# Performance work log

Measured on AMD Instinct MI355X. Metric: run time of the kernel, lower is better.

The kernel has to match this reference:

```python
import jax, jax.numpy as jnp
import numpy as np

EPS = 1e-5
K_NBR = 21   # num_neighbors + 1 (self)
PSI = 4


def _bn(x, g, b):
    # BatchNorm (training-mode forward): channel-last, normalize over all other axes
    axes = tuple(range(x.ndim - 1))
    m = jnp.mean(x, axis=axes, keepdims=True)
    v = jnp.var(x, axis=axes, keepdims=True)
    return (x - m) * jax.lax.rsqrt(v + EPS) * g + b


def setup_inputs() -> dict:
    key = jax.random.key(0)
    ks = jax.random.split(key, 16)
    B, N, Cin, Cout = 4, 2048, 64, 256
    h = Cout // 2
    w_ch = Cout // PSI
    heads = 2 * PSI - 1

    def w(k, o, i):
        return jax.random.normal(k, (o, i), dtype=jnp.float32) * (1.0 / np.sqrt(i))

    p = {}
    p['xyz'] = jax.random.normal(ks[0], (B, N, 3), dtype=jnp.float32)
    p['f'] = jax.random.normal(ks[1], (B, Cin, N), dtype=jnp.float32)
    p['W_geo'] = w(ks[2], h, 6);       p['g_geo'] = jnp.ones(h);   p['b_geo'] = jnp.zeros(h)
    p['W_feat'] = w(ks[3], h, 2 * Cin); p['g_feat'] = jnp.ones(h); p['b_feat'] = jnp.zeros(h)
    p['g_bn'] = jnp.ones(Cout); p['b_bn'] = jnp.zeros(Cout)
    p['W_q'] = w(ks[4], Cout, Cout); p['g_q'] = jnp.ones(Cout); p['b_q'] = jnp.zeros(Cout)
    p['W_k'] = w(ks[5], Cout, Cout); p['g_k'] = jnp.ones(Cout); p['b_k'] = jnp.zeros(Cout)
    p['W_v'] = w(ks[6], Cout, Cout); p['g_v'] = jnp.ones(Cout); p['b_v'] = jnp.zeros(Cout)
    p['W_fus'] = w(ks[7], Cout, heads * w_ch); p['bias_fus'] = jnp.zeros(Cout)
    p['g_fus'] = jnp.ones(Cout); p['b_fus'] = jnp.zeros(Cout)
    p['g_ln'] = jnp.ones(Cout); p['b_ln'] = jnp.zeros(Cout)
    p['W_mlp'] = w(ks[8], Cout, Cout); p['bias_mlp'] = jnp.zeros(Cout)
    return p


def reference(xyz, f, W_geo, g_geo, b_geo, W_feat, g_feat, b_feat, g_bn, b_bn,
              W_q, g_q, b_q, W_k, g_k, b_k, W_v, g_v, b_v,
              W_fus, bias_fus, g_fus, b_fus, g_ln, b_ln, W_mlp, bias_mlp):
    B, N, _ = xyz.shape
    Cout = g_bn.shape[0]
    w_ch = Cout // PSI
    d_sh = w_ch // 2
    heads = 2 * PSI - 1

    # ---- PositionFusion: KNN grouping ----
    sq = jnp.sum(xyz * xyz, axis=-1)                                   # [B,N]
    d2 = sq[:, :, None] + sq[:, None, :] - 2.0 * jnp.einsum('bnd,bmd->bnm', xyz, xyz)
    _, idx = jax.lax.top_k(-d2, K_NBR)                                 # [B,N,K]

    grouped_xyz = jax.vmap(lambda p, i: p[i])(xyz, idx)                # [B,N,K,3]
    xyz_diff = grouped_xyz - xyz[:, :, None, :]
    geo_in = jnp.concatenate(
        [jnp.broadcast_to(xyz[:, :, None, :], grouped_xyz.shape), xyz_diff], axis=-1)  # [B,N,K,6]

    ft = jnp.transpose(f, (0, 2, 1))                                   # [B,N,Cin]
    grouped_f = jax.vmap(lambda p, i: p[i])(ft, idx)                   # [B,N,K,Cin]
    feat_in = jnp.concatenate(
        [grouped_f, jnp.broadcast_to(ft[:, :, None, :], grouped_f.shape)], axis=-1)    # [B,N,K,2Cin]

    geo = jax.nn.relu(_bn(jnp.einsum('bnki,oi->bnko', geo_in, W_geo), g_geo, b_geo))
    fea = jax.nn.relu(_bn(jnp.einsum('bnki,oi->bnko', feat_in, W_feat), g_feat, b_feat))
    feature_ = jnp.max(jnp.concatenate([geo, fea], axis=-1), axis=2)   # [B,N,Cout] (maxpool over K)

    # ---- BatchNorm1d ----
    x = _bn(feature_, g_bn, b_bn)

    # ---- Shifted-channel multi-head attention ----
    q = jax.nn.relu(_bn(jnp.einsum('bnc,oc->bno', x, W_q), g_q, b_q))
    k = jax.nn.relu(_bn(jnp.einsum('bnc,oc->bno', x, W_k), g_k, b_k))
    v = jax.nn.relu(_bn(jnp.einsum('bnc,oc->bno', x, W_v), g_v, b_v))

    qh = jnp.stack([q[..., m * d_sh:m * d_sh + w_ch] for m in range(heads)], axis=1)  # [B,H,N,w]
    kh = jnp.stack([k[..., m * d_sh:m * d_sh + w_ch] for m in range(heads)], axis=1)
    vh = jnp.stack([v[..., m * d_sh:m * d_sh + w_ch] for m in range(heads)], axis=1)

    a = jax.nn.softmax(jnp.einsum('bhnc,bhmc->bhnm', qh, kh), axis=-1)  # [B,H,N,N]
    o = jnp.einsum('bhnm,bhmc->bhnc', a, vh)                            # [B,H,N,w]
    O = jnp.transpose(o, (0, 2, 1, 3)).reshape(B, N, heads * w_ch)      # channel-concat per head

    fus = jax.nn.relu(_bn(jnp.einsum('bnc,oc->bno', O, W_fus) + bias_fus, g_fus, b_fus))

    feature__ = fus + feature_                                          # residual

    # ---- LayerNorm over channels ----
    m = jnp.mean(feature__, axis=-1, keepdims=True)
    var = jnp.var(feature__, axis=-1, keepdims=True)
    y = (feature__ - m) * jax.lax.rsqrt(var + EPS) * g_ln + b_ln

    out = feature__ + (jnp.einsum('bnc,oc->bno', y, W_mlp) + bias_mlp)
    return jnp.transpose(out, (0, 2, 1))                                # [B,Cout,N] like torch
```

## Files before the change

kernel.cpp:

```cpp
#include <hip/hip_runtime.h>
#include <math.h>

#define NB    4
#define NPTS  2048
#define ROWS  (NB*NPTS)
#define CIN   64
#define COUT  256
#define KNBR  21
#define NHEADS 7
#define WCH   64
#define DSH   32
#define LOG2E 1.4426950408889634f
#define KLD   72

typedef __attribute__((ext_vector_type(8))) short short8;
typedef __attribute__((ext_vector_type(4))) float floatx4;

#if __has_builtin(__builtin_amdgcn_exp2f)
#define EXP2(x) __builtin_amdgcn_exp2f(x)
#else
#define EXP2(x) __expf((x)*0.6931471805599453f)
#endif
#if __has_builtin(__builtin_amdgcn_rcpf)
#define RCP(x) __builtin_amdgcn_rcpf(x)
#else
#define RCP(x) (1.0f/(x))
#endif

__device__ __forceinline__ ushort f2bf(float x) {
    unsigned u = __float_as_uint(x);
    u += 0x7fffu + ((u >> 16) & 1u);
    return (ushort)(u >> 16);
}

__device__ __forceinline__ float bf2f(short u) {
    return __uint_as_float(((unsigned)(unsigned short)u) << 16);
}

__device__ __forceinline__ unsigned cvt_pk_bf16(float lo, float hi) {
    unsigned r;
    asm("v_cvt_pk_bf16_f32 %0, %1, %2" : "=v"(r) : "v"(lo), "v"(hi));
    return r;
}

template<int CTRL, int RMASK>
__device__ __forceinline__ unsigned dpp_umin_step(unsigned x) {
    unsigned t = (unsigned)__builtin_amdgcn_update_dpp((int)x, (int)x, CTRL, RMASK, 0xF, false);
    return (t < x) ? t : x;
}
__device__ __forceinline__ unsigned wave_min_u32(unsigned x) {
    x = dpp_umin_step<0x111, 0xF>(x);
    x = dpp_umin_step<0x112, 0xF>(x);
    x = dpp_umin_step<0x114, 0xF>(x);
    x = dpp_umin_step<0x118, 0xF>(x);
    x = dpp_umin_step<0x142, 0xA>(x);
    x = dpp_umin_step<0x143, 0xC>(x);
    return (unsigned)__builtin_amdgcn_readlane((int)x, 63);
}

__device__ __forceinline__ unsigned umin2(unsigned a, unsigned b) { return a < b ? a : b; }
__device__ __forceinline__ unsigned umax2(unsigned a, unsigned b) { return a < b ? b : a; }

__device__ __forceinline__ void ins6(unsigned &m1, unsigned &m2, unsigned &m3,
                                     unsigned &m4, unsigned &m5, unsigned &m6, unsigned k) {
    unsigned c = k, t;
    t = umin2(m1, c); c = umax2(m1, c); m1 = t;
    t = umin2(m2, c); c = umax2(m2, c); m2 = t;
    t = umin2(m3, c); c = umax2(m3, c); m3 = t;
    t = umin2(m4, c); c = umax2(m4, c); m4 = t;
    t = umin2(m5, c); c = umax2(m5, c); m5 = t;
    m6 = umin2(m6, c);
}

__global__ __launch_bounds__(256) void prep_knn(const float* __restrict__ f, const float* __restrict__ Wf,
                                                const float* __restrict__ xyz, const float* __restrict__ Wg,
                                                const float* __restrict__ W_q, const float* __restrict__ W_k,
                                                const float* __restrict__ W_v, const float* __restrict__ W_fus,
                                                float* __restrict__ X, float* __restrict__ A,
                                                ushort* __restrict__ Wb, float* __restrict__ sums,
                                                int* __restrict__ idx) {
    __shared__ float4 SXQ[2048];
    int t = threadIdx.x;
    int blk = blockIdx.x;
    if (blk < 512) {
        float* As = (float*)SXQ;
        float* Ws = As + 16*68;
        int bx = blk & 127, by = blk >> 7;
        if (by == 0 && bx < 12) sums[bx*256 + t] = 0.f;
        int gid = (by*128 + bx)*256 + t;
        for (int i = gid; i < 311296; i += 131072) {
            const float* Wsrc; int off;
            if (i < 65536)       { Wsrc = W_q;   off = i; }
            else if (i < 131072) { Wsrc = W_k;   off = i - 65536; }
            else if (i < 196608) { Wsrc = W_v;   off = i - 131072; }
            else                 { Wsrc = W_fus; off = i - 196608; }
            Wb[i] = f2bf(Wsrc[off]);
        }
        int r0 = bx * 64, n0 = by * 64;
        for (int e = t; e < 4096; e += 256) {
            int row = r0 + (e >> 6), c = n0 + (e & 63), cc = c & 127;
            float x = xyz[row*3], y = xyz[row*3+1], z = xyz[row*3+2];
            const float* w = Wg + cc*6;
            float s = (c < 128) ? ((w[3]*x + w[4]*y) + w[5]*z)
                                : (((w[0]-w[3])*x + (w[1]-w[4])*y) + (w[2]-w[5])*z);
            A[(size_t)row*256 + c] = s;
        }
        int b = r0 >> 11, nbase = r0 & 2047;
        int tx = t & 15, ty = t >> 4;
        float acc[4][4];
#pragma unroll
        for (int i = 0; i < 4; i++)
#pragma unroll
            for (int j = 0; j < 4; j++) acc[i][j] = 0.f;
        int m64 = t & 63, kg = t >> 6;
        int lk = t & 15, lm = t >> 4;
        for (int k0 = 0; k0 < 64; k0 += 16) {
#pragma unroll
            for (int p = 0; p < 4; p++) {
                int k = kg*4 + p;
                As[k*68 + m64] = f[(size_t)b*CIN*NPTS + (size_t)(k0 + k)*NPTS + nbase + m64];
            }
#pragma unroll
            for (int i2 = 0; i2 < 4; i2++) {
                int cg = n0 + lm + 16*i2;
                Ws[lk*68 + lm + 16*i2] = Wf[(size_t)(cg & 127)*128 + (cg >> 7)*64 + k0 + lk];
            }
            __syncthreads();
#pragma unroll
            for (int kq = 0; kq < 16; kq++) {
                float4 a  = *(const float4*)&As[kq*68 + 4*ty];
                float4 b4 = *(const float4*)&Ws[kq*68 + 4*tx];
                float av[4] = {a.x, a.y, a.z, a.w};
                float bv[4] = {b4.x, b4.y, b4.z, b4.w};
#pragma unroll
                for (int i = 0; i < 4; i++)
#pragma unroll
                    for (int j = 0; j < 4; j++) acc[i][j] = fmaf(av[i], bv[j], acc[i][j]);
            }
            __syncthreads();
        }
#pragma unroll
        for (int i = 0; i < 4; i++)
#pragma unroll
            for (int j = 0; j < 4; j++)
                X[(size_t)(r0 + 4*ty + i)*256 + n0 + 4*tx + j] = acc[i][j];
        return;
    }
    int kb = blk - 512;
    int b = kb >> 9;
    int g = kb & 511;
    for (int m = t; m < NPTS; m += 256) {
        float x = xyz[(size_t)b*NPTS*3 + m*3];
        float y = xyz[(size_t)b*NPTS*3 + m*3 + 1];
        float z = xyz[(size_t)b*NPTS*3 + m*3 + 2];
        SXQ[m] = make_float4(x, y, z, (x*x + y*y) + z*z);
    }
    __syncthreads();
    int w = t >> 6, lane = t & 63;
    int n = g*4 + w;
    float4 q4 = SXQ[n];
    float qx = q4.x, qy = q4.y, qz = q4.z, sqn = q4.w;

    unsigned key[32];
    unsigned a1 = 0xFFFFFFFFu, a2 = 0xFFFFFFFFu, a3 = 0xFFFFFFFFu,
             a4 = 0xFFFFFFFFu, a5 = 0xFFFFFFFFu, a6 = 0xFFFFFFFFu;
    unsigned c1 = 0xFFFFFFFFu, c2 = 0xFFFFFFFFu, c3 = 0xFFFFFFFFu,
             c4 = 0xFFFFFFFFu, c5 = 0xFFFFFFFFu, c6 = 0xFFFFFFFFu;
#pragma unroll
    for (int i = 0; i < 16; i++) {
        int m = lane + (i << 6);
        float4 p = SXQ[m];
        float dt = (qx*p.x + qy*p.y) + qz*p.z;
        float d2 = fmaxf((sqn + p.w) - 2.0f*dt, 0.f);
        unsigned kv = (__float_as_uint(d2) & 0xFFFFF800u) | (unsigned)m;
        key[i] = kv;
        ins6(a1, a2, a3, a4, a5, a6, kv);
    }
#pragma unroll
    for (int i = 16; i < 32; i++) {
        int m = lane + (i << 6);
        float4 p = SXQ[m];
        float dt = (qx*p.x + qy*p.y) + qz*p.z;
        float d2 = fmaxf((sqn + p.w) - 2.0f*dt, 0.f);
        unsigned kv = (__float_as_uint(d2) & 0xFFFFF800u) | (unsigned)m;
        key[i] = kv;
        ins6(c1, c2, c3, c4, c5, c6, kv);
    }
    ins6(a1, a2, a3, a4, a5, a6, c1);
    ins6(a1, a2, a3, a4, a5, a6, c2);
    ins6(a1, a2, a3, a4, a5, a6, c3);
    ins6(a1, a2, a3, a4, a5, a6, c4);
    ins6(a1, a2, a3, a4, a5, a6, c5);
    ins6(a1, a2, a3, a4, a5, a6, c6);

    unsigned winkey = 0xFFFFFFFFu;
    {
        unsigned fr = a1, p2 = a2, p3 = a3, p4 = a4, p5 = a5, p6 = a6;
#pragma unroll
        for (int kk = 0; kk < 32; kk++) {
            unsigned win = wave_min_u32(fr);
            if (lane == kk) winkey = win;
            bool own = (fr == win);
            fr = own ? p2 : fr;
            p2 = own ? p3 : p2;
            p3 = own ? p4 : p3;
            p4 = own ? p5 : p4;
            p5 = own ? p6 : p5;
            p6 = own ? 0xFFFFFFFFu : p6;
        }
        if (__ballot(fr == 0xFFFFFFFFu) != 0ULL) {
            winkey = 0xFFFFFFFFu;
            for (int kk = 0; kk < 32; kk++) {
                unsigned lv = key[0];
#pragma unroll
                for (int i = 1; i < 32; i++) lv = (key[i] < lv) ? key[i] : lv;
                unsigned win = wave_min_u32(lv);
                if (lane == kk) winkey = win;
                unsigned widx = win & 2047u;
                int slot = (int)(widx >> 6);
                bool own = (lane == (int)(widx & 63u));
#pragma unroll
                for (int i = 0; i < 32; i++)
                    if (i == slot && own) key[i] = 0xFFFFFFFFu;
            }
        }
    }
    double d2r;
    int mr;
    {
        double qx64 = (double)qx, qy64 = (double)qy, qz64 = (double)qz;
        double sqn64 = qx64*qx64 + qy64*qy64 + qz64*qz64;
        if (lane < 32) {
            mr = (int)(winkey & 2047u);
            float4 p = SXQ[mr];
            double x = (double)p.x, y = (double)p.y, z = (double)p.z;
            double sqm = x*x + y*y + z*z;
            double dt  = qx64*x + qy64*y + qz64*z;
            d2r = (sqn64 + sqm) - 2.0*dt;
        } else {
            d2r = INFINITY; mr = 0x7FFFFFFF;
        }
    }
#pragma unroll
    for (int k = 2; k <= 32; k <<= 1) {
#pragma unroll
        for (int j = k >> 1; j > 0; j >>= 1) {
            double od = __shfl_xor(d2r, j, 64);
            int    om = __shfl_xor(mr, j, 64);
            bool up    = ((lane & k) == 0);
            bool lower = ((lane & j) == 0);
            bool oless = (od < d2r) || (od == d2r && om < mr);
            bool keepOther = up ? (lower ? oless : !oless) : (lower ? !oless : oless);
            if (keepOther) { d2r = od; mr = om; }
        }
    }
    if (lane < KNBR)
        idx[((size_t)b*NPTS + n)*KNBR + lane] = mr;
}

__global__ __launch_bounds__(256) void stats_gf(const float* __restrict__ geoBC, const float* __restrict__ featAC,
                                                const int* __restrict__ idx, const float* __restrict__ g_geo,
                                                const float* __restrict__ g_feat,
                                                float* __restrict__ sums, float* __restrict__ xsel) {
    int c = threadIdx.x;
    int cc = c & 127;
    const float* base = (c < 128) ? geoBC : featAC;
    bool wantmax = ((c < 128) ? g_geo[cc] : g_feat[cc]) >= 0.f;
    float s = 0.f, ss = 0.f;
    int r0 = blockIdx.x * 32;
    for (int r = r0; r < r0 + 32; r++) {
        int b = r >> 11;
        float ctr = base[(size_t)r*256 + 128 + cc];
        float mx = -1e30f, mn = 1e30f;
        const int* ip = idx + (size_t)r*KNBR;
        for (int kk = 0; kk < KNBR; kk++) {
            int j = ip[kk];
            float xv = ctr + base[((size_t)(b*NPTS + j))*256 + cc];
            mx = fmaxf(mx, xv); mn = fminf(mn, xv);
            s += xv; ss += xv*xv;
        }
        xsel[(size_t)r*256 + c] = wantmax ? mx : mn;
    }
    atomicAdd(&sums[c], s);
    atomicAdd(&sums[256 + c], ss);
}

__global__ __launch_bounds__(256) void feature_maxsel(const float* __restrict__ xsel, const float* __restrict__ sums,
                                                      const float* __restrict__ g_geo, const float* __restrict__ b_geo,
                                                      const float* __restrict__ g_feat, const float* __restrict__ b_feat,
                                                      float* __restrict__ feat, float* __restrict__ sums_bn1) {
    int c = threadIdx.x;
    const float inv = 1.0f / (float)(ROWS*KNBR);
    float mean = sums[c]*inv;
    float var  = sums[256+c]*inv - mean*mean;
    float g  = (c < 128) ? g_geo[c] : g_feat[c-128];
    float bb = (c < 128) ? b_geo[c] : b_feat[c-128];
    float sc = g / sqrtf(var + 1e-5f);
    float tt = bb - mean*sc;
    float s = 0.f, ss = 0.f;
    int r0 = blockIdx.x*32;
    for (int r = r0; r < r0+32; r++) {
        size_t i = (size_t)r*256 + c;
        float y = fmaxf(fmaf(sc, xsel[i], tt), 0.f);
        feat[i] = y; s += y; ss += y*y;
    }
    atomicAdd(&sums_bn1[c], s); atomicAdd(&sums_bn1[256+c], ss);
}

__global__ __launch_bounds__(256) void gemm_qkv(const float* __restrict__ Af, const float* __restrict__ sums_in,
                                                const float* __restrict__ g_bn, const float* __restrict__ b_bn,
                                                const ushort* __restrict__ Wb,
                                                float* __restrict__ QKVF, float* __restrict__ sums) {
    __shared__ float bns[2][256];
    __shared__ float red[4][256][2];
    int t = threadIdx.x;
    int r0 = blockIdx.x * 64, g = blockIdx.y;
    int w = t >> 6, lane = t & 63;
    int r15 = lane & 15, quad = lane >> 4;
    {
        float mean = sums_in[512 + t] * (1.0f/(float)ROWS);
        float var  = sums_in[768 + t] * (1.0f/(float)ROWS) - mean*mean;
        float sc = g_bn[t] / sqrtf(var + 1e-5f);
        bns[0][t] = sc;
        bns[1][t] = b_bn[t] - mean*sc;
    }
    __syncthreads();
    short8 aq[8];
    {
        const float* ap = Af + (size_t)(r0 + 16*w + r15)*256;
#pragma unroll
        for (int kc = 0; kc < 8; kc++) {
            int k0 = 32*kc + 8*quad;
            float4 a0 = *(const float4*)&ap[k0];
            float4 a1 = *(const float4*)&ap[k0+4];
            float4 s0 = *(const float4*)&bns[0][k0];
            float4 s1 = *(const float4*)&bns[0][k0+4];
            float4 h0 = *(const float4*)&bns[1][k0];
            float4 h1 = *(const float4*)&bns[1][k0+4];
            ushort u8[8];
            u8[0] = f2bf(fmaf(s0.x, a0.x, h0.x)); u8[1] = f2bf(fmaf(s0.y, a0.y, h0.y));
            u8[2] = f2bf(fmaf(s0.z, a0.z, h0.z)); u8[3] = f2bf(fmaf(s0.w, a0.w, h0.w));
            u8[4] = f2bf(fmaf(s1.x, a1.x, h1.x)); u8[5] = f2bf(fmaf(s1.y, a1.y, h1.y));
            u8[6] = f2bf(fmaf(s1.z, a1.z, h1.z)); u8[7] = f2bf(fmaf(s1.w, a1.w, h1.w));
            aq[kc] = *(short8*)u8;
        }
    }
    floatx4 zero4 = {0.f, 0.f, 0.f, 0.f};
    floatx4 acc[16];
#pragma unroll
    for (int st = 0; st < 16; st++) acc[st] = zero4;
    const ushort* wbase = Wb + (size_t)g*65536 + (size_t)r15*256 + 8*quad;
#pragma unroll
    for (int st = 0; st < 16; st++) {
        const ushort* wp = wbase + (size_t)(16*st)*256;
#pragma unroll
        for (int kc = 0; kc < 8; kc++) {
            short8 bf = *(const short8*)(wp + 32*kc);
            acc[st] = __builtin_amdgcn_mfma_f32_16x16x32_bf16(aq[kc], bf, acc[st], 0, 0, 0);
        }
    }
#pragma unroll
    for (int st = 0; st < 16; st++) {
        float s  = (acc[st][0] + acc[st][1]) + (acc[st][2] + acc[st][3]);
        float q2 = (acc[st][0]*acc[st][0] + acc[st][1]*acc[st][1]) +
                   (acc[st][2]*acc[st][2] + acc[st][3]*acc[st][3]);
        s  += __shfl_xor(s, 16, 64);  s  += __shfl_xor(s, 32, 64);
        q2 += __shfl_xor(q2, 16, 64); q2 += __shfl_xor(q2, 32, 64);
        if (lane < 16) { red[w][16*st + r15][0] = s; red[w][16*st + r15][1] = q2; }
#pragma unroll
        for (int reg = 0; reg < 4; reg++)
            QKVF[(size_t)(r0 + 16*w + 4*quad + reg)*768 + g*256 + 16*st + r15] = acc[st][reg];
    }
    __syncthreads();
    {
        float s = red[0][t][0] + red[1][t][0] + red[2][t][0] + red[3][t][0];
        float q = red[0][t][1] + red[1][t][1] + red[2][t][1] + red[3][t][1];
        atomicAdd(&sums[1024 + g*512 + t], s);
        atomicAdd(&sums[1024 + g*512 + 256 + t], q);
    }
}

__global__ __launch_bounds__(256) void affine_qkv(const float* __restrict__ QKVF, const float* __restrict__ sums,
                                                  const float* __restrict__ g_q, const float* __restrict__ b_q,
                                                  const float* __restrict__ g_k, const float* __restrict__ b_k,
                                                  const float* __restrict__ g_v, const float* __restrict__ b_v,
                                                  ushort* __restrict__ qk, ushort* __restrict__ vt) {
    __shared__ float sts[6][256];
    __shared__ ushort tile[64][72];
    int t = threadIdx.x;
    {
        const float* gs[3] = {g_q, g_k, g_v};
        const float* bs[3] = {b_q, b_k, b_v};
#pragma unroll
        for (int g = 0; g < 3; g++) {
            float mean = sums[1024 + g*512 + t] * (1.0f/(float)ROWS);
            float var  = sums[1024 + g*512 + 256 + t] * (1.0f/(float)ROWS) - mean*mean;
            float sc = gs[g][t] / sqrtf(var + 1e-5f);
            float sh = bs[g][t] - mean*sc;
            if (g == 0) { sc *= LOG2E; sh *= LOG2E; }
            sts[2*g][t] = sc;
            sts[2*g+1][t] = sh;
        }
    }
    __syncthreads();
    int r0 = blockIdx.x * 64, c0 = blockIdx.y * 64;
    int b = r0 >> 11, nbase = r0 & 2047;
    if (c0 < 512) {
#pragma unroll
        for (int rep = 0; rep < 16; rep++) {
            int e = t + 256*rep;
            int row = e >> 6, c = e & 63;
            int col = c0 + c, g = col >> 8, cc = col & 255;
            float v = QKVF[(size_t)(r0 + row)*768 + col];
            v = fmaxf(fmaf(sts[2*g][cc], v, sts[2*g+1][cc]), 0.f);
            qk[(size_t)(r0 + row)*512 + col] = f2bf(v);
        }
    } else {
#pragma unroll
        for (int rep = 0; rep < 16; rep++) {
            int e = t + 256*rep;
            int row = e >> 6, c = e & 63;
            int col = c0 + c, cc = col & 255;
            float v = QKVF[(size_t)(r0 + row)*768 + col];
            v = fmaxf(fmaf(sts[4][cc], v, sts[5][cc]), 0.f);
            tile[c][row] = f2bf(v);
        }
        __syncthreads();
#pragma unroll
        for (int rep = 0; rep < 16; rep++) {
            int e = t + 256*rep;
            int cc = e >> 6, nn = e & 63;
            vt[((size_t)(b*256 + (c0 - 512) + cc))*2048 + nbase + nn] = tile[cc][nn];
        }
    }
}

__global__ __launch_bounds__(512) void attn2(const ushort* __restrict__ qk, const ushort* __restrict__ vt,
                                             ushort* __restrict__ obp, float* __restrict__ ml) {
    __shared__ ushort Ksh[2][64*KLD];
    __shared__ ushort Vts[2][64*KLD];
    int h = blockIdx.y;
    int z = blockIdx.z, b = z >> 1, half = z & 1;
    int r0 = blockIdx.x * 128;
    int t = threadIdx.x;
    int w = t >> 6, lane = t & 63;
    int r15 = lane & 15, quad = lane >> 4;
    size_t rowbase = (size_t)b*NPTS;
    int hoff = h*DSH;
    int rr = t >> 3, c8 = t & 7;
    int mstart = half << 10, mend = mstart + 1024;

    const ushort* ksrc = qk + (rowbase + rr)*512 + 256 + hoff + 8*c8;
    const ushort* vsrc = vt + ((size_t)(b*256 + hoff + rr))*2048 + 8*c8;
    int ldstK = rr*KLD + 8*c8;
    int vb = 4*((c8 >> 1) & 1) + 16*(c8 & 1) + 32*(c8 >> 2);
    int ldstV = rr*KLD + vb;

    short8 aq[2];
#pragma unroll
    for (int s = 0; s < 2; s++)
        aq[s] = *(const short8*)(qk + (rowbase + r0 + 16*w + r15)*512 + hoff + 32*s + 8*quad);

    {
        uint4 k0 = *(const uint4*)(ksrc + (size_t)mstart*512);
        uint4 v0 = *(const uint4*)(vsrc + mstart);
        *(uint4*)&Ksh[0][ldstK] = k0;
        *(uint2*)&Vts[0][ldstV]     = make_uint2(v0.x, v0.y);
        *(uint2*)&Vts[0][ldstV + 8] = make_uint2(v0.z, v0.w);
    }

    floatx4 zero4 = {0.f, 0.f, 0.f, 0.f};
    floatx4 oacc[4];
    float mrun = -1e30f, lrun = 0.f;
#pragma unroll
    for (int i = 0; i < 4; i++) oacc[i] = zero4;

    asm volatile("s_waitcnt lgkmcnt(0)" ::: "memory");
    __builtin_amdgcn_s_barrier();
    __builtin_amdgcn_sched_barrier(0);

    int cur = 0;
    for (int m0 = mstart; m0 < mend; m0 += 64) {
        int mnext = (m0 + 64 < mend) ? (m0 + 64) : mstart;
        uint4 kreg = *(const uint4*)(ksrc + (size_t)mnext*512);
        uint4 vreg = *(const uint4*)(vsrc + mnext);

        const ushort* Kc = Ksh[cur];
        const ushort* Vc = Vts[cur];

        floatx4 sacc[4];
#pragma unroll
        for (int tt = 0; tt < 4; tt++) sacc[tt] = zero4;
        __builtin_amdgcn_s_setprio(1);
#pragma unroll
        for (int tt = 0; tt < 4; tt++) {
            int key = 16*tt + r15;
#pragma unroll
            for (int s = 0; s < 2; s++) {
                short8 kf = *(const short8*)&Kc[key*KLD + 32*s + 8*quad];
                sacc[tt] = __builtin_amdgcn_mfma_f32_16x16x32_bf16(kf, aq[s], sacc[tt], 0, 0, 0);
            }
        }
        __builtin_amdgcn_s_setprio(0);

        float mx = sacc[0][0];
#pragma unroll
        for (int tt = 0; tt < 4; tt++)
#pragma unroll
            for (int reg = 0; reg < 4; reg++) mx = fmaxf(mx, sacc[tt][reg]);
        mx = fmaxf(mx, __shfl_xor(mx, 16, 64));
        mx = fmaxf(mx, __shfl_xor(mx, 32, 64));

        if (!__all(mx <= mrun)) {
            float mnew = fmaxf(mrun, mx);
            float alpha = EXP2(mrun - mnew);
            lrun *= alpha;
#pragma unroll
            for (int td = 0; td < 4; td++) oacc[td] *= alpha;
            mrun = mnew;
        }

        float pm[4][4];
        float rs = 0.f;
#pragma unroll
        for (int tt = 0; tt < 4; tt++) {
#pragma unroll
            for (int reg = 0; reg < 4; reg++) {
                float p = EXP2(sacc[tt][reg] - mrun);
                pm[tt][reg] = p; rs += p;
            }
        }
        rs += __shfl_xor(rs, 16, 64);
        rs += __shfl_xor(rs, 32, 64);
        lrun += rs;

        uint4 pk0, pk1;
        pk0.x = cvt_pk_bf16(pm[0][0], pm[0][1]); pk0.y = cvt_pk_bf16(pm[0][2], pm[0][3]);
        pk0.z = cvt_pk_bf16(pm[1][0], pm[1][1]); pk0.w = cvt_pk_bf16(pm[1][2], pm[1][3]);
        pk1.x = cvt_pk_bf16(pm[2][0], pm[2][1]); pk1.y = cvt_pk_bf16(pm[2][2], pm[2][3]);
        pk1.z = cvt_pk_bf16(pm[3][0], pm[3][1]); pk1.w = cvt_pk_bf16(pm[3][2], pm[3][3]);
        short8 pf0 = *(short8*)&pk0;
        short8 pf1 = *(short8*)&pk1;

        __builtin_amdgcn_s_setprio(1);
#pragma unroll
        for (int td = 0; td < 4; td++) {
            short8 vf0 = *(const short8*)&Vc[(16*td + r15)*KLD + 8*quad];
            oacc[td] = __builtin_amdgcn_mfma_f32_16x16x32_bf16(vf0, pf0, oacc[td], 0, 0, 0);
            short8 vf1 = *(const short8*)&Vc[(16*td + r15)*KLD + 32 + 8*quad];
            oacc[td] = __builtin_amdgcn_mfma_f32_16x16x32_bf16(vf1, pf1, oacc[td], 0, 0, 0);
        }
        __builtin_amdgcn_s_setprio(0);

        *(uint4*)&Ksh[cur ^ 1][ldstK] = kreg;
        *(uint2*)&Vts[cur ^ 1][ldstV]     = make_uint2(vreg.x, vreg.y);
        *(uint2*)&Vts[cur ^ 1][ldstV + 8] = make_uint2(vreg.z, vreg.w);
        cur ^= 1;

        asm volatile("s_waitcnt lgkmcnt(0)" ::: "memory");
        __builtin_amdgcn_s_barrier();
        __builtin_amdgcn_sched_barrier(0);
    }

    size_t grow = rowbase + r0 + 16*w + r15;
    ushort* op = obp + (size_t)half*((size_t)ROWS*448) + grow*448 + h*WCH;
#pragma unroll
    for (int td = 0; td < 4; td++) {
        uint2 o2;
        o2.x = cvt_pk_bf16(oacc[td][0], oacc[td][1]);
        o2.y = cvt_pk_bf16(oacc[td][2], oacc[td][3]);
        *(uint2*)&op[16*td + 4*quad] = o2;
    }
    if (quad == 0) {
        *(float2*)&ml[(grow*7 + h)*4 + half*2] = make_float2(mrun, lrun);
    }
}

__global__ __launch_bounds__(256) void gemm_fus(const ushort* __restrict__ OBP, const float* __restrict__ ML,
                                                const ushort* __restrict__ Wb,
                                                const float* __restrict__ bias, float* __restrict__ C,
                                                float* __restrict__ sums) {
    __shared__ float red[4][128][2];
    int t = threadIdx.x;
    int r0 = blockIdx.x * 64, n0 = blockIdx.y * 128;
    int w = t >> 6, lane = t & 63;
    int r15 = lane & 15, quad = lane >> 4;
    int arow = 16*w + r15;
    short8 aq[14];
    {
        const ushort* p1 = OBP + (size_t)(r0 + arow)*448;
        const ushort* p2 = p1 + (size_t)ROWS*448;
        const float* mlr = ML + (size_t)(r0 + arow)*28;
        float w1[7], w2[7];
#pragma unroll
        for (int hh = 0; hh < 7; hh++) {
            float m1 = mlr[hh*4+0], l1 = mlr[hh*4+1];
            float m2 = mlr[hh*4+2], l2 = mlr[hh*4+3];
            float M  = fmaxf(m1, m2);
            float e1 = EXP2(m1 - M), e2 = EXP2(m2 - M);
            float inv = RCP(fmaf(e1, l1, e2*l2));
            w1[hh] = e1*inv; w2[hh] = e2*inv;
        }
#pragma unroll
        for (int kc = 0; kc < 14; kc++) {
            int k0 = 32*kc + 8*quad;
            short8 a1 = *(const short8*)(p1 + k0);
            short8 a2 = *(const short8*)(p2 + k0);
            const int hh = kc >> 1;
            float c0 = fmaf(w1[hh], bf2f(a1[0]), w2[hh]*bf2f(a2[0]));
            float c1 = fmaf(w1[hh], bf2f(a1[1]), w2[hh]*bf2f(a2[1]));
            float c2 = fmaf(w1[hh], bf2f(a1[2]), w2[hh]*bf2f(a2[2]));
            float c3 = fmaf(w1[hh], bf2f(a1[3]), w2[hh]*bf2f(a2[3]));
            float c4 = fmaf(w1[hh], bf2f(a1[4]), w2[hh]*bf2f(a2[4]));
            float c5 = fmaf(w1[hh], bf2f(a1[5]), w2[hh]*bf2f(a2[5]));
            float c6 = fmaf(w1[hh], bf2f(a1[6]), w2[hh]*bf2f(a2[6]));
            float c7 = fmaf(w1[hh], bf2f(a1[7]), w2[hh]*bf2f(a2[7]));
            uint4 pk;
            pk.x = cvt_pk_bf16(c0, c1); pk.y = cvt_pk_bf16(c2, c3);
            pk.z = cvt_pk_bf16(c4, c5); pk.w = cvt_pk_bf16(c6, c7);
            aq[kc] = *(short8*)&pk;
        }
    }
    floatx4 zero4 = {0.f, 0.f, 0.f, 0.f};
    floatx4 acc[8];
#pragma unroll
    for (int st = 0; st < 8; st++) acc[st] = zero4;
    const ushort* wbase = Wb + 196608 + (size_t)(n0 + r15)*448 + 8*quad;
#pragma unroll
    for (int st = 0; st < 8; st++) {
        const ushort* wp = wbase + (size_t)(16*st)*448;
#pragma unroll
        for (int kc = 0; kc < 14; kc++) {
            short8 bf = *(const short8*)(wp + 32*kc);
            acc[st] = __builtin_amdgcn_mfma_f32_16x16x32_bf16(aq[kc], bf, acc[st], 0, 0, 0);
        }
    }
#pragma unroll
    for (int st = 0; st < 8; st++) {
        int col = n0 + 16*st + r15;
        float bi = bias[col];
        float v0 = acc[st][0] + bi, v1 = acc[st][1] + bi, v2 = acc[st][2] + bi, v3 = acc[st][3] + bi;
        float s  = (v0 + v1) + (v2 + v3);
        float q2 = (v0*v0 + v1*v1) + (v2*v2 + v3*v3);
        s  += __shfl_xor(s, 16, 64);  s  += __shfl_xor(s, 32, 64);
        q2 += __shfl_xor(q2, 16, 64); q2 += __shfl_xor(q2, 32, 64);
        if (lane < 16) { red[w][16*st + r15][0] = s; red[w][16*st + r15][1] = q2; }
        C[(size_t)(r0 + 16*w + 4*quad + 0)*256 + col] = v0;
        C[(size_t)(r0 + 16*w + 4*quad + 1)*256 + col] = v1;
        C[(size_t)(r0 + 16*w + 4*quad + 2)*256 + col] = v2;
        C[(size_t)(r0 + 16*w + 4*quad + 3)*256 + col] = v3;
    }
    __syncthreads();
    {
        int col = t >> 1, which = t & 1;
        float v = red[0][col][which] + red[1][col][which] + red[2][col][which] + red[3][col][which];
        atomicAdd(&sums[2560 + which*256 + n0 + col], v);
    }
}

__global__ __launch_bounds__(256) void gemm_mlp_ln(const float* __restrict__ FUSP, const float* __restrict__ A,
                                                   const float* __restrict__ sums,
                                                   const float* __restrict__ g_fus, const float* __restrict__ b_fus,
                                                   const float* __restrict__ g_ln, const float* __restrict__ b_ln,
                                                   const float* __restrict__ W, const float* __restrict__ bias,
                                                   float* __restrict__ outp) {
    __shared__ float Ys[256][68];
    __shared__ float FFs[64][65];
    __shared__ float Ws[16][68];
    __shared__ float tr[64][65];
    __shared__ float SC[256], SH[256], GL[256], BL[256];
    int t = threadIdx.x;
    int r0 = blockIdx.x*64, n0 = blockIdx.y*64;
    {
        float mean0 = sums[2560 + t] * (1.0f/(float)ROWS);
        float var0  = sums[2560 + 256 + t] * (1.0f/(float)ROWS) - mean0*mean0;
        float sc = g_fus[t] / sqrtf(var0 + 1e-5f);
        SC[t] = sc; SH[t] = b_fus[t] - mean0*sc;
        GL[t] = g_ln[t]; BL[t] = b_ln[t];
    }
    __syncthreads();
    int row = t >> 2, seg = t & 3;
    size_t rb = (size_t)(r0 + row)*256;
    float4 vv[16];
    float s = 0.f, ss = 0.f;
#pragma unroll
    for (int j = 0; j < 16; j++) {
        int c = seg*64 + 4*j;
        float4 fp = *(const float4*)&FUSP[rb + c];
        float4 fe = *(const float4*)&A[rb + c];
        float4 sc4 = *(const float4*)&SC[c];
        float4 sh4 = *(const float4*)&SH[c];
        float4 v;
        v.x = fmaxf(fmaf(sc4.x, fp.x, sh4.x), 0.f) + fe.x;
        v.y = fmaxf(fmaf(sc4.y, fp.y, sh4.y), 0.f) + fe.y;
        v.z = fmaxf(fmaf(sc4.z, fp.z, sh4.z), 0.f) + fe.z;
        v.w = fmaxf(fmaf(sc4.w, fp.w, sh4.w), 0.f) + fe.w;
        vv[j] = v;
        s  += (v.x + v.y) + (v.z + v.w);
        ss += (v.x*v.x + v.y*v.y) + (v.z*v.z + v.w*v.w);
        if (seg == blockIdx.y) *(float4*)&FFs[row][4*j] = v;
    }
    s  += __shfl_xor(s, 1, 64);  s  += __shfl_xor(s, 2, 64);
    ss += __shfl_xor(ss, 1, 64); ss += __shfl_xor(ss, 2, 64);
    float mean = s * (1.f/256.f);
    float var  = ss * (1.f/256.f) - mean*mean;
    float rin  = 1.f/sqrtf(var + 1e-5f);
#pragma unroll
    for (int j = 0; j < 16; j++) {
        int c = seg*64 + 4*j;
        float4 gl = *(const float4*)&GL[c];
        float4 bl = *(const float4*)&BL[c];
        float4 v = vv[j];
        Ys[c+0][row] = (v.x - mean)*rin*gl.x + bl.x;
        Ys[c+1][row] = (v.y - mean)*rin*gl.y + bl.y;
        Ys[c+2][row] = (v.z - mean)*rin*gl.z + bl.z;
        Ys[c+3][row] = (v.w - mean)*rin*gl.w + bl.w;
    }
    __syncthreads();
    int tx = t & 15, ty = t >> 4;
    int lk = t & 15, lm = t >> 4;
    float acc[4][4];
#pragma unroll
    for (int i = 0; i < 4; i++)
#pragma unroll
        for (int j = 0; j < 4; j++) acc[i][j] = 0.f;
    for (int k0 = 0; k0 < 256; k0 += 16) {
#pragma unroll
        for (int i2 = 0; i2 < 4; i2++)
            Ws[lk][lm + 16*i2] = W[(size_t)(n0 + lm + 16*i2)*256 + k0 + lk];
        __syncthreads();
#pragma unroll
        for (int kq = 0; kq < 16; kq++) {
            float4 a  = *(const float4*)&Ys[k0 + kq][4*ty];
            float4 b4 = *(const float4*)&Ws[kq][4*tx];
            float av[4] = {a.x, a.y, a.z, a.w};
            float bv[4] = {b4.x, b4.y, b4.z, b4.w};
#pragma unroll
            for (int i = 0; i < 4; i++)
#pragma unroll
                for (int j = 0; j < 4; j++) acc[i][j] = fmaf(av[i], bv[j], acc[i][j]);
        }
        __syncthreads();
    }
#pragma unroll
    for (int i = 0; i < 4; i++)
#pragma unroll
        for (int j = 0; j < 4; j++) {
            float v = acc[i][j] + bias[n0 + 4*tx + j] + FFs[4*ty + i][4*tx + j];
            tr[4*tx + j][4*ty + i] = v;
        }
    __syncthreads();
    int b = r0 >> 11, nbase = r0 & 2047;
#pragma unroll
    for (int rep = 0; rep < 16; rep++) {
        int e = t + 256*rep;
        int cl = e >> 6, nl = e & 63;
        outp[((size_t)(b*256 + n0 + cl))*2048 + nbase + nl] = tr[cl][nl];
    }
}

extern "C" void kernel_launch(void* const* d_in, const int* in_sizes, int n_in,
                              void* d_out, int out_size, void* d_ws, size_t ws_size,
                              hipStream_t stream) {
    const float* xyz    = (const float*)d_in[0];
    const float* f      = (const float*)d_in[1];
    const float* W_geo  = (const float*)d_in[2];
    const float* g_geo  = (const float*)d_in[3];
    const float* b_geo  = (const float*)d_in[4];
    const float* W_feat = (const float*)d_in[5];
    const float* g_feat = (const float*)d_in[6];
    const float* b_feat = (const float*)d_in[7];
    const float* g_bn   = (const float*)d_in[8];
    const float* b_bn   = (const float*)d_in[9];
    const float* W_q    = (const float*)d_in[10];
    const float* g_q    = (const float*)d_in[11];
    const float* b_q    = (const float*)d_in[12];
    const float* W_k    = (const float*)d_in[13];
    const float* g_k    = (const float*)d_in[14];
    const float* b_k    = (const float*)d_in[15];
    const float* W_v    = (const float*)d_in[16];
    const float* g_v    = (const float*)d_in[17];
    const float* b_v    = (const float*)d_in[18];
    const float* W_fus  = (const float*)d_in[19];
    const float* bias_fus = (const float*)d_in[20];
    const float* g_fus  = (const float*)d_in[21];
    const float* b_fus  = (const float*)d_in[22];
    const float* g_ln   = (const float*)d_in[23];
    const float* b_ln   = (const float*)d_in[24];
    const float* W_mlp  = (const float*)d_in[25];
    const float* bias_mlp = (const float*)d_in[26];

    float* ws = (float*)d_ws;
    const size_t MBF = 262144;
    float* SUMS  = ws;
    int*   IDX   = (int*)(ws + 16384);
    float* A     = ws + 1*MBF;
    float* X     = ws + 9*MBF;
    ushort* QK16 = (ushort*)(ws + 9*MBF);
    float* FUSP  = ws + 9*MBF;
    float* CSEL  = ws + 17*MBF;
    float* QKVF  = ws + 17*MBF;
    ushort* OBP  = (ushort*)(ws + 17*MBF);
    float* ML    = ws + 33*MBF;
    ushort* VT16 = (ushort*)(ws + 45*MBF);
    ushort* WB16 = (ushort*)(ws + 49*MBF);

    prep_knn<<<2560, 256, 0, stream>>>(f, W_feat, xyz, W_geo, W_q, W_k, W_v, W_fus,
                                       X, A, WB16, SUMS, IDX);
    stats_gf<<<256, 256, 0, stream>>>(A, X, IDX, g_geo, g_feat, SUMS, CSEL);
    feature_maxsel<<<256, 256, 0, stream>>>(CSEL, SUMS, g_geo, b_geo, g_feat, b_feat, A, SUMS + 512);
    gemm_qkv<<<dim3(128, 3), 256, 0, stream>>>(A, SUMS, g_bn, b_bn, WB16, QKVF, SUMS);
    affine_qkv<<<dim3(128, 12), 256, 0, stream>>>(QKVF, SUMS, g_q, b_q, g_k, b_k, g_v, b_v, QK16, VT16);
    attn2<<<dim3(NPTS/128, NHEADS, NB*2), 512, 0, stream>>>(QK16, VT16, OBP, ML);
    gemm_fus<<<dim3(128, 2), 256, 0, stream>>>(OBP, ML, WB16, bias_fus, FUSP, SUMS);
    gemm_mlp_ln<<<dim3(128, 4), 256, 0, stream>>>(FUSP, A, SUMS, g_fus, b_fus, g_ln, b_ln,
                                                  W_mlp, bias_mlp, (float*)d_out);
}
```

Baseline: 372.9 us.

## Process two query row tiles per wave in attention to reuse K/V fragments

Each wave in the attention kernel now handles 32 query rows (two 16-row tiles) instead of 16, so every K and V fragment loaded from shared memory feeds two MFMAs. Block rows double to 256 and the grid halves along x. This aims to cut LDS traffic and the K/V staging and barrier overhead per unit of work. In exchange it raises register pressure (doubled accumulators) and reduces the block count to 448, which may lower occupancy or leave CUs idle.

```diff
diff --git a/kernel.cpp b/kernel.cpp
--- a/kernel.cpp
+++ b/kernel.cpp
@@ -441,7 +441,7 @@
     __shared__ ushort Vts[2][64*KLD];
     int h = blockIdx.y;
     int z = blockIdx.z, b = z >> 1, half = z & 1;
-    int r0 = blockIdx.x * 128;
+    int r0 = blockIdx.x * 256;
     int t = threadIdx.x;
     int w = t >> 6, lane = t & 63;
     int r15 = lane & 15, quad = lane >> 4;
@@ -456,10 +456,12 @@
     int vb = 4*((c8 >> 1) & 1) + 16*(c8 & 1) + 32*(c8 >> 2);
     int ldstV = rr*KLD + vb;
 
-    short8 aq[2];
-#pragma unroll
-    for (int s = 0; s < 2; s++)
-        aq[s] = *(const short8*)(qk + (rowbase + r0 + 16*w + r15)*512 + hoff + 32*s + 8*quad);
+    short8 aq[2][2];
+#pragma unroll
+    for (int u = 0; u < 2; u++)
+#pragma unroll
+        for (int s = 0; s < 2; s++)
+            aq[u][s] = *(const short8*)(qk + (rowbase + r0 + 32*w + 16*u + r15)*512 + hoff + 32*s + 8*quad);
 
     {
         uint4 k0 = *(const uint4*)(ksrc + (size_t)mstart*512);
@@ -470,10 +472,14 @@
     }
 
     floatx4 zero4 = {0.f, 0.f, 0.f, 0.f};
-    floatx4 oacc[4];
-    float mrun = -1e30f, lrun = 0.f;
-#pragma unroll
-    for (int i = 0; i < 4; i++) oacc[i] = zero4;
+    floatx4 oacc[2][4];
+    float mrun[2], lrun[2];
+#pragma unroll
+    for (int u = 0; u < 2; u++) {
+        mrun[u] = -1e30f; lrun[u] = 0.f;
+#pragma unroll
+        for (int i = 0; i < 4; i++) oacc[u][i] = zero4;
+    }
 
     asm volatile("s_waitcnt lgkmcnt(0)" ::: "memory");
     __builtin_amdgcn_s_barrier();
@@ -488,9 +494,11 @@
         const ushort* Kc = Ksh[cur];
         const ushort* Vc = Vts[cur];
 
-        floatx4 sacc[4];
-#pragma unroll
-        for (int tt = 0; tt < 4; tt++) sacc[tt] = zero4;
+        floatx4 sacc[2][4];
+#pragma unroll
+        for (int u = 0; u < 2; u++)
+#pragma unroll
+            for (int tt = 0; tt < 4; tt++) sacc[u][tt] = zero4;
         __builtin_amdgcn_s_setprio(1);
 #pragma unroll
         for (int tt = 0; tt < 4; tt++) {
@@ -498,57 +506,64 @@
 #pragma unroll
             for (int s = 0; s < 2; s++) {
                 short8 kf = *(const short8*)&Kc[key*KLD + 32*s + 8*quad];
-                sacc[tt] = __builtin_amdgcn_mfma_f32_16x16x32_bf16(kf, aq[s], sacc[tt], 0, 0, 0);
+                sacc[0][tt] = __builtin_amdgcn_mfma_f32_16x16x32_bf16(kf, aq[0][s], sacc[0][tt], 0, 0, 0);
+                sacc[1][tt] = __builtin_amdgcn_mfma_f32_16x16x32_bf16(kf, aq[1][s], sacc[1][tt], 0, 0, 0);
             }
         }
         __builtin_amdgcn_s_setprio(0);
 
-        float mx = sacc[0][0];
-#pragma unroll
-        for (int tt = 0; tt < 4; tt++)
-#pragma unroll
-            for (int reg = 0; reg < 4; reg++) mx = fmaxf(mx, sacc[tt][reg]);
-        mx = fmaxf(mx, __shfl_xor(mx, 16, 64));
-        mx = fmaxf(mx, __shfl_xor(mx, 32, 64));
-
-        if (!__all(mx <= mrun)) {
-            float mnew = fmaxf(mrun, mx);
-            float alpha = EXP2(mrun - mnew);
-            lrun *= alpha;
-#pragma unroll
-            for (int td = 0; td < 4; td++) oacc[td] *= alpha;
-            mrun = mnew;
-        }
-
-        float pm[4][4];
-        float rs = 0.f;
-#pragma unroll
-        for (int tt = 0; tt < 4; tt++) {
-#pragma unroll
-            for (int reg = 0; reg < 4; reg++) {
-                float p = EXP2(sacc[tt][reg] - mrun);
-                pm[tt][reg] = p; rs += p;
+        short8 pf[2][2];
+#pragma unroll
+        for (int u = 0; u < 2; u++) {
+            float mx = sacc[u][0][0];
+#pragma unroll
+            for (int tt = 0; tt < 4; tt++)
+#pragma unroll
+                for (int reg = 0; reg < 4; reg++) mx = fmaxf(mx, sacc[u][tt][reg]);
+            mx = fmaxf(mx, __shfl_xor(mx, 16, 64));
+            mx = fmaxf(mx, __shfl_xor(mx, 32, 64));
+
+            if (!__all(mx <= mrun[u])) {
+                float mnew = fmaxf(mrun[u], mx);
+                float alpha = EXP2(mrun[u] - mnew);
+                lrun[u] *= alpha;
+#pragma unroll
+                for (int td = 0; td < 4; td++) oacc[u][td] *= alpha;
+                mrun[u] = mnew;
             }
-        }
-        rs += __shfl_xor(rs, 16, 64);
-        rs += __shfl_xor(rs, 32, 64);
-        lrun += rs;
-
-        uint4 pk0, pk1;
-        pk0.x = cvt_pk_bf16(pm[0][0], pm[0][1]); pk0.y = cvt_pk_bf16(pm[0][2], pm[0][3]);
-        pk0.z = cvt_pk_bf16(pm[1][0], pm[1][1]); pk0.w = cvt_pk_bf16(pm[1][2], pm[1][3]);
-        pk1.x = cvt_pk_bf16(pm[2][0], pm[2][1]); pk1.y = cvt_pk_bf16(pm[2][2], pm[2][3]);
-        pk1.z = cvt_pk_bf16(pm[3][0], pm[3][1]); pk1.w = cvt_pk_bf16(pm[3][2], pm[3][3]);
-        short8 pf0 = *(short8*)&pk0;
-        short8 pf1 = *(short8*)&pk1;
+
+            float pm[4][4];
+            float rs = 0.f;
+#pragma unroll
+            for (int tt = 0; tt < 4; tt++) {
+#pragma unroll
+                for (int reg = 0; reg < 4; reg++) {
+                    float p = EXP2(sacc[u][tt][reg] - mrun[u]);
+                    pm[tt][reg] = p; rs += p;
+                }
+            }
+            rs += __shfl_xor(rs, 16, 64);
+            rs += __shfl_xor(rs, 32, 64);
+            lrun[u] += rs;
+
+            uint4 pk0, pk1;
+            pk0.x = cvt_pk_bf16(pm[0][0], pm[0][1]); pk0.y = cvt_pk_bf16(pm[0][2], pm[0][3]);
+            pk0.z = cvt_pk_bf16(pm[1][0], pm[1][1]); pk0.w = cvt_pk_bf16(pm[1][2], pm[1][3]);
+            pk1.x = cvt_pk_bf16(pm[2][0], pm[2][1]); pk1.y = cvt_pk_bf16(pm[2][2], pm[2][3]);
+            pk1.z = cvt_pk_bf16(pm[3][0], pm[3][1]); pk1.w = cvt_pk_bf16(pm[3][2], pm[3][3]);
+            pf[u][0] = *(short8*)&pk0;
+            pf[u][1] = *(short8*)&pk1;
+        }
 
         __builtin_amdgcn_s_setprio(1);
 #pragma unroll
         for (int td = 0; td < 4; td++) {
             short8 vf0 = *(const short8*)&Vc[(16*td + r15)*KLD + 8*quad];
-            oacc[td] = __builtin_amdgcn_mfma_f32_16x16x32_bf16(vf0, pf0, oacc[td], 0, 0, 0);
+            oacc[0][td] = __builtin_amdgcn_mfma_f32_16x16x32_bf16(vf0, pf[0][0], oacc[0][td], 0, 0, 0);
+            oacc[1][td] = __builtin_amdgcn_mfma_f32_16x16x32_bf16(vf0, pf[1][0], oacc[1][td], 0, 0, 0);
             short8 vf1 = *(const short8*)&Vc[(16*td + r15)*KLD + 32 + 8*quad];
-            oacc[td] = __builtin_amdgcn_mfma_f32_16x16x32_bf16(vf1, pf1, oacc[td], 0, 0, 0);
+            oacc[0][td] = __builtin_amdgcn_mfma_f32_16x16x32_bf16(vf1, pf[0][1], oacc[0][td], 0, 0, 0);
+            oacc[1][td] = __builtin_amdgcn_mfma_f32_16x16x32_bf16(vf1, pf[1][1], oacc[1][td], 0, 0, 0);
         }
         __builtin_amdgcn_s_setprio(0);
 
@@ -562,17 +577,20 @@
         __builtin_amdgcn_sched_barrier(0);
     }
 
-    size_t grow = rowbase + r0 + 16*w + r15;
-    ushort* op = obp + (size_t)half*((size_t)ROWS*448) + grow*448 + h*WCH;
-#pragma unroll
-    for (int td = 0; td < 4; td++) {
-        uint2 o2;
-        o2.x = cvt_pk_bf16(oacc[td][0], oacc[td][1]);
-        o2.y = cvt_pk_bf16(oacc[td][2], oacc[td][3]);
-        *(uint2*)&op[16*td + 4*quad] = o2;
-    }
-    if (quad == 0) {
-        *(float2*)&ml[(grow*7 + h)*4 + half*2] = make_float2(mrun, lrun);
+#pragma unroll
+    for (int u = 0; u < 2; u++) {
+        size_t grow = rowbase + r0 + 32*w + 16*u + r15;
+        ushort* op = obp + (size_t)half*((size_t)ROWS*448) + grow*448 + h*WCH;
+#pragma unroll
+        for (int td = 0; td < 4; td++) {
+            uint2 o2;
+            o2.x = cvt_pk_bf16(oacc[u][td][0], oacc[u][td][1]);
+            o2.y = cvt_pk_bf16(oacc[u][td][2], oacc[u][td][3]);
+            *(uint2*)&op[16*td + 4*quad] = o2;
+        }
+        if (quad == 0) {
+            *(float2*)&ml[(grow*7 + h)*4 + half*2] = make_float2(mrun[u], lrun[u]);
+        }
     }
 }
 
@@ -811,7 +829,7 @@
     feature_maxsel<<<256, 256, 0, stream>>>(CSEL, SUMS, g_geo, b_geo, g_feat, b_feat, A, SUMS + 512);
     gemm_qkv<<<dim3(128, 3), 256, 0, stream>>>(A, SUMS, g_bn, b_bn, WB16, QKVF, SUMS);
     affine_qkv<<<dim3(128, 12), 256, 0, stream>>>(QKVF, SUMS, g_q, b_q, g_k, b_k, g_v, b_v, QK16, VT16);
-    attn2<<<dim3(NPTS/128, NHEADS, NB*2), 512, 0, stream>>>(QK16, VT16, OBP, ML);
+    attn2<<<dim3(NPTS/256, NHEADS, NB*2), 512, 0, stream>>>(QK16, VT16, OBP, ML);
     gemm_fus<<<dim3(128, 2), 256, 0, stream>>>(OBP, ML, WB16, bias_fus, FUSP, SUMS);
     gemm_mlp_ln<<<dim3(128, 4), 256, 0, stream>>>(FUSP, A, SUMS, g_fus, b_fus, g_ln, b_ln,
                                                   W_mlp, bias_mlp, (float*)d_out);
```

Measured after the change: 372.0 us. About the same (-0.2%).
